# Kernel tuning notes

Hardware: AMD Instinct MI355X
Metric: run time of the kernel (lower is better)

The kernel has to match this reference:

```python
import jax, jax.numpy as jnp
import numpy as np

EPS = 1e-15
PROJ_EPS = 4e-3  # standard Poincare-ball projection epsilon (float32)


def _logmap0(x, c):
    sqrt_c = jnp.sqrt(c)
    norm = jnp.maximum(jnp.linalg.norm(x, axis=-1, keepdims=True), EPS)
    arg = jnp.clip(sqrt_c * norm, -1.0 + EPS, 1.0 - EPS)
    return x / (sqrt_c * norm) * jnp.arctanh(arg)


def _expmap0(u, c):
    sqrt_c = jnp.sqrt(c)
    norm = jnp.maximum(jnp.linalg.norm(u, axis=-1, keepdims=True), EPS)
    return jnp.tanh(sqrt_c * norm) * u / (sqrt_c * norm)


def _proj(x, c):
    maxnorm = (1.0 - PROJ_EPS) / jnp.sqrt(c)
    norm = jnp.maximum(jnp.linalg.norm(x, axis=-1, keepdims=True), EPS)
    return jnp.where(norm > maxnorm, x * (maxnorm / norm), x)


def setup_inputs() -> dict:
    key = jax.random.key(0)
    k1, k2, k3, k4 = jax.random.split(key, 4)
    N, E, F = 50000, 800000, 96
    # points strictly inside the Poincare ball
    x = 0.01 * jax.random.normal(k1, (N, F), dtype=jnp.float32)
    edge_index = jax.random.randint(k2, (2, E), 0, N, dtype=jnp.int64)
    W_up = jax.random.normal(k3, (F, F), dtype=jnp.float32) * (1.0 / np.sqrt(F))
    W_lw = jax.random.normal(k4, (1, 2 * F), dtype=jnp.float32) * (1.0 / np.sqrt(2 * F))
    return {"x": x, "edge_index": edge_index, "W_up": W_up, "W_lw": W_lw}


def reference(x, edge_index, W_up, W_lw):
    c = 1.0
    N = x.shape[0]
    row, col = edge_index[0], edge_index[1]  # source j -> target i

    x_tan = _logmap0(x, c)

    # NodeInformationScore: out = (I - D^{-1/2} A D^{-1/2}) x_tan
    ew = jnp.ones(row.shape[0], dtype=x.dtype)
    deg = jax.ops.segment_sum(ew, row, num_segments=N)
    dinv = jnp.where(deg > 0, deg, 1.0) ** -0.5
    dinv = jnp.where(deg > 0, dinv, 0.0)
    norm_e = -dinv[row] * ew * dinv[col]  # edge coefficients; self-loop coeff = 1
    info = jax.ops.segment_sum(norm_e[:, None] * x_tan[row], col, num_segments=N) + x_tan
    score = jnp.sum(jnp.abs(info), axis=1)  # [N]

    updated = jax.nn.leaky_relu(x_tan @ W_up.T, 0.01)  # [N, F]
    sum_neigh = jax.ops.segment_sum(updated[row], col, num_segments=N)

    sel = (score > 1.0).astype(x.dtype)[:, None]  # hot_prob / SEL_v
    sum_sel = jax.ops.segment_sum((sel * updated)[row], col, num_segments=N)

    w_sel = jax.nn.sigmoid(jnp.concatenate([sum_sel, sum_neigh], axis=-1) @ W_lw.T)  # [N,1]
    A_x = jax.nn.relu(jax.ops.segment_sum((w_sel * sel * updated)[row], col, num_segments=N))

    out = updated + A_x
    return _proj(_expmap0(out, c), c)
```

## Files before the change

### kernel.cpp

```cpp
#include <hip/hip_runtime.h>
#include <math.h>

#define FDIM 96
#define CAP 64
#define CAPB 5120
#define EB 8192
#define BLCAP 2048
#define T2MAX 768

typedef float f4 __attribute__((ext_vector_type(4)));
typedef unsigned u32x3 __attribute__((ext_vector_type(3)));

static __device__ __forceinline__ float wave_sum(float v) {
    for (int off = 32; off; off >>= 1) v += __shfl_xor(v, off, 64);
    return v;
}
static __device__ __forceinline__ float half_sum(float v) {
    for (int off = 16; off; off >>= 1) v += __shfl_xor(v, off, 64);
    return v;
}
static __device__ __forceinline__ float grp_sum(float v) {
    v += __shfl_xor(v, 1, 64);
    v += __shfl_xor(v, 2, 64);
    v += __shfl_xor(v, 4, 64);
    return v;
}
static __device__ __forceinline__ float bf_lo(unsigned u) { return __uint_as_float(u << 16); }
static __device__ __forceinline__ float bf_hi(unsigned u) { return __uint_as_float(u & 0xffff0000u); }
static __device__ __forceinline__ unsigned bf_rne(float f) {
    unsigned x = __float_as_uint(f);
    return (x + 0x7fffu + ((x >> 16) & 1u)) >> 16;
}
static __device__ __forceinline__ unsigned f_to_f8(float f) {
    union { _Float16 h; unsigned short u; } c;
    c.h = (_Float16)f;
    unsigned b = (unsigned)c.u + 0x80u;
    return (b >> 8) & 0xffu;
}
static __device__ __forceinline__ float f8h(unsigned hb) {
    union { unsigned short u; _Float16 h; } c;
    c.u = (unsigned short)hb;
    return (float)c.h;
}
static __device__ __forceinline__ float dot4(f4 a) {
    return a.x * a.x + a.y * a.y + a.z * a.z + a.w * a.w;
}

__global__ __launch_bounds__(512) void k_bucket_gemm(
    const int* __restrict__ row, const int* __restrict__ col,
    const float* __restrict__ x, const float* __restrict__ W,
    unsigned* __restrict__ stageC, unsigned char* __restrict__ stageR,
    int* __restrict__ fillC, int* __restrict__ fillR,
    unsigned char* __restrict__ xfb8, unsigned* __restrict__ upb,
    int n, int E, int Gbkt, int t2)
{
    __shared__ __align__(16) char shmem[FDIM * 100 * 4 + 64 * FDIM * 2];
    int t = threadIdx.x;

    if ((int)blockIdx.x < Gbkt) {
        unsigned* stC = (unsigned*)shmem;
        unsigned char* stR = (unsigned char*)(shmem + EB * 4);
        int* histC = (int*)(shmem + EB * 5);
        int* histR = histC + 256;
        int* baseC = histR + 256;
        int* baseR = baseC + 256;
        int* gbC   = baseR + 256;
        int* gbR   = gbC + 256;
        if (t < 256) { histC[t] = 0; histR[t] = 0; }
        __syncthreads();
        int e0 = (int)blockIdx.x * EB;
        unsigned pk[16];
#pragma unroll
        for (int u = 0; u < 16; ++u) {
            int e = e0 + t + u * 512;
            if (e < E) {
                unsigned c = (unsigned)col[e], r = (unsigned)row[e];
                pk[u] = (c << 16) | r;
                atomicAdd(&histC[c >> 8], 1);
                atomicAdd(&histR[r >> 8], 1);
            } else pk[u] = 0xffffffffu;
        }
        __syncthreads();
        if (t < 256) { baseC[t] = histC[t]; baseR[t] = histR[t]; }
        __syncthreads();
        for (int ofs = 1; ofs < 256; ofs <<= 1) {
            int vc = 0, vr = 0;
            if (t < 256 && t >= ofs) { vc = baseC[t - ofs]; vr = baseR[t - ofs]; }
            __syncthreads();
            if (t < 256 && t >= ofs) { baseC[t] += vc; baseR[t] += vr; }
            __syncthreads();
        }
        if (t < 256) {
            baseC[t] -= histC[t];  baseR[t] -= histR[t];
            gbC[t] = histC[t] ? atomicAdd(&fillC[t], histC[t]) : 0;
            gbR[t] = histR[t] ? atomicAdd(&fillR[t], histR[t]) : 0;
        }
        __syncthreads();
#pragma unroll
        for (int u = 0; u < 16; ++u) {
            if (pk[u] != 0xffffffffu) {
                int bc = pk[u] >> 24;
                int br = (pk[u] >> 8) & 0xff;
                int p  = atomicAdd(&baseC[bc], 1);
                stC[p] = pk[u];
                int p2 = atomicAdd(&baseR[br], 1);
                stR[p2] = (unsigned char)(pk[u] & 0xffu);
            }
        }
        __syncthreads();
        int wv = t >> 6, ln = t & 63;
        for (int b = wv; b < 256; b += 8) {
            int lenC = histC[b];
            if (lenC) {
                int s0 = baseC[b] - lenC;
                int room = CAPB - gbC[b]; if (room < 0) room = 0;
                int lim = lenC < room ? lenC : room;
                unsigned* g = stageC + (size_t)b * CAPB + gbC[b];
                for (int k = ln; k < lim; k += 64) g[k] = stC[s0 + k];
            }
            int lenR = histR[b];
            if (lenR) {
                int s1 = baseR[b] - lenR;
                int room = CAPB - gbR[b]; if (room < 0) room = 0;
                int lim = lenR < room ? lenR : room;
                unsigned char* g = stageR + (size_t)b * CAPB + gbR[b];
                for (int k = ln; k < lim; k += 64) g[k] = stR[s1 + k];
            }
        }
        return;
    }

    float* Wsf = (float*)shmem;
    unsigned short* xsb = (unsigned short*)(shmem + FDIM * 100 * 4);
    unsigned* xsb32 = (unsigned*)xsb;
    for (int idx = t; idx < FDIM * FDIM; idx += 512)
        Wsf[(idx / FDIM) * 100 + (idx % FDIM)] = W[idx];
    __syncthreads();
    int tiles = (n + 63) / 64;
    int r0 = t >> 5, c = t & 31;
    for (int tile = (int)blockIdx.x - Gbkt; tile < tiles; tile += t2) {
        int row0 = tile * 64;
#pragma unroll
        for (int rr = 0; rr < 4; ++rr) {
            int lr = r0 + rr * 16;
            int gr = row0 + lr;
            float v0 = 0.f, v1 = 0.f, v2 = 0.f;
            if (gr < n) {
                const float* xr = x + (size_t)gr * FDIM;
                v0 = xr[c]; v1 = xr[c + 32]; v2 = xr[c + 64];
            }
            float ss = half_sum(v0 * v0 + v1 * v1 + v2 * v2);
            float norm = fmaxf(sqrtf(ss), 1e-15f);
            float s = atanhf(fminf(norm, 1.0f)) / norm;
            xsb[lr * FDIM + c]      = (unsigned short)bf_rne(v0 * s);
            xsb[lr * FDIM + c + 32] = (unsigned short)bf_rne(v1 * s);
            xsb[lr * FDIM + c + 64] = (unsigned short)bf_rne(v2 * s);
        }
        __syncthreads();
        for (int idx = t; idx < 64 * 24; idx += 512) {
            int r2 = idx / 24, wq = idx % 24, g = row0 + r2;
            if (g < n) {
                unsigned p0 = xsb32[r2 * 48 + wq * 2];
                unsigned p1 = xsb32[r2 * 48 + wq * 2 + 1];
                unsigned o = f_to_f8(bf_lo(p0)) | (f_to_f8(bf_hi(p0)) << 8)
                           | (f_to_f8(bf_lo(p1)) << 16) | (f_to_f8(bf_hi(p1)) << 24);
                ((unsigned*)xfb8)[(size_t)g * 24 + wq] = o;
            }
        }
        float acc[4][3];
#pragma unroll
        for (int rr = 0; rr < 4; ++rr) { acc[rr][0] = 0.f; acc[rr][1] = 0.f; acc[rr][2] = 0.f; }
#pragma unroll 6
        for (int q = 0; q < 24; ++q) {
            f4 w0 = *(const f4*)&Wsf[c * 100 + q * 4];
            f4 w1 = *(const f4*)&Wsf[(c + 32) * 100 + q * 4];
            f4 w2 = *(const f4*)&Wsf[(c + 64) * 100 + q * 4];
#pragma unroll
            for (int rr = 0; rr < 4; ++rr) {
                uint2 xv = *(const uint2*)&xsb32[(r0 + rr * 16) * 48 + q * 2];
                float x0 = bf_lo(xv.x), x1 = bf_hi(xv.x);
                float x2 = bf_lo(xv.y), x3 = bf_hi(xv.y);
                acc[rr][0] = fmaf(x0, w0.x, fmaf(x1, w0.y, fmaf(x2, w0.z, fmaf(x3, w0.w, acc[rr][0]))));
                acc[rr][1] = fmaf(x0, w1.x, fmaf(x1, w1.y, fmaf(x2, w1.z, fmaf(x3, w1.w, acc[rr][1]))));
                acc[rr][2] = fmaf(x0, w2.x, fmaf(x1, w2.y, fmaf(x2, w2.z, fmaf(x3, w2.w, acc[rr][2]))));
            }
        }
        __syncthreads();
#pragma unroll
        for (int rr = 0; rr < 4; ++rr) {
            int lr = r0 + rr * 16;
            float a0 = acc[rr][0], a1 = acc[rr][1], a2 = acc[rr][2];
            a0 = a0 > 0.f ? a0 : 0.01f * a0;
            a1 = a1 > 0.f ? a1 : 0.01f * a1;
            a2 = a2 > 0.f ? a2 : 0.01f * a2;
            xsb[lr * FDIM + c]      = (unsigned short)bf_rne(a0);
            xsb[lr * FDIM + c + 32] = (unsigned short)bf_rne(a1);
            xsb[lr * FDIM + c + 64] = (unsigned short)bf_rne(a2);
        }
        __syncthreads();
        for (int idx = t; idx < 64 * 48; idx += 512) {
            int r2 = idx / 48, cc = idx % 48, g = row0 + r2;
            if (g < n) upb[(size_t)g * 48 + cc] = xsb32[r2 * 48 + cc];
        }
        __syncthreads();
    }
}

__global__ __launch_bounds__(512) void k_csr_deg(
    const unsigned* __restrict__ stageC, const unsigned char* __restrict__ stageR,
    const int* __restrict__ fillC, const int* __restrict__ fillR,
    float* __restrict__ dinv, int* __restrict__ cnt, unsigned short* __restrict__ srcp,
    int n, int nbuck)
{
    __shared__ __align__(16) char shmem[1024 + 256 * CAP * 2];
    int t = threadIdx.x;
    int bid = (int)blockIdx.x;

    if (bid < nbuck) {
        int* hist = (int*)shmem;
        unsigned short* comp = (unsigned short*)(shmem + 1024);
        if (t < 256) hist[t] = 0;
        __syncthreads();
        int nb = fillC[bid]; if (nb > CAPB) nb = CAPB;
        const unsigned* sc = stageC + (size_t)bid * CAPB;
        for (int k = t; k < nb; k += 512) {
            unsigned pk = sc[k];
            int cl = (pk >> 16) & 255;
            int slot = atomicAdd(&hist[cl], 1);
            if (slot < CAP) comp[cl * CAP + slot] = (unsigned short)(pk & 0xffffu);
        }
        __syncthreads();
        int node0 = bid << 8;
        if (t < 256 && node0 + t < n) cnt[node0 + t] = hist[t];
        int nnode = n - node0; if (nnode > 256) nnode = 256;
        if (nnode > 0) {
            int lim32 = nnode * (CAP / 2);
            unsigned* dst = (unsigned*)(srcp + (size_t)node0 * CAP);
            const unsigned* src = (const unsigned*)comp;
            for (int k = t; k < lim32; k += 512) dst[k] = src[k];
        }
        return;
    }
    int b = bid - nbuck;
    int* hist = (int*)shmem;
    if (t < 256) hist[t] = 0;
    __syncthreads();
    int nb = fillR[b]; if (nb > CAPB) nb = CAPB;
    const unsigned char* sr = stageR + (size_t)b * CAPB;
    for (int k = t; k < nb; k += 512) atomicAdd(&hist[sr[k]], 1);
    __syncthreads();
    int node0 = b << 8;
    if (t < 256 && node0 + t < n) {
        int d = hist[t];
        dinv[node0 + t] = d > 0 ? (float)(1.0 / sqrt((double)d)) : 0.f;
    }
}

#define DEC4(w, cf, A, B, C, D)                              \
    A = fmaf(cf, f8h(((w) & 0xffu) << 8), A);                \
    B = fmaf(cf, f8h((w) & 0xff00u), B);                     \
    C = fmaf(cf, f8h(((w) >> 8) & 0xff00u), C);              \
    D = fmaf(cf, f8h(((w) >> 16) & 0xff00u), D);

__global__ __launch_bounds__(256) void k_pass1(
    const float* __restrict__ x, const unsigned char* __restrict__ xfb8,
    const unsigned short* __restrict__ srcp, const int* __restrict__ cnt,
    const float* __restrict__ dinv, float* __restrict__ sel,
    int* __restrict__ blist, int* __restrict__ nbl, int n)
{
    int t = threadIdx.x;
    int lane = t & 63;
    int gid = lane >> 3, gl = lane & 7;
    int grp = lane & 56;
    int node = (int)blockIdx.x * 32 + (t >> 6) * 8 + gid;
    int nd = node < n ? node : 0;
    int m = cnt[nd];
    if (m > CAP) m = CAP;
    if (node >= n) m = 0;
    float di = dinv[nd];
    int jreg[8]; float cfreg[8];
#pragma unroll
    for (int s = 0; s < 8; ++s) {
        int k = s * 8 + gl;
        int j = (k < m) ? (int)srcp[(size_t)nd * CAP + k] : 0;
        jreg[s] = j;
        cfreg[s] = (k < m) ? -di * dinv[j] : 0.f;
    }
    const f4* xr = (const f4*)(x + (size_t)nd * FDIM + gl * 12);
    f4 o0 = xr[0], o1 = xr[1], o2 = xr[2];
    float ns = grp_sum(dot4(o0) + dot4(o1) + dot4(o2));
    float no = fmaxf(sqrtf(ns), 1e-15f);
    float so = atanhf(fminf(no, 1.0f)) / no;
    float a0 = o0.x*so, a1 = o0.y*so, a2 = o0.z*so, a3 = o0.w*so;
    float a4 = o1.x*so, a5 = o1.y*so, a6 = o1.z*so, a7 = o1.w*so;
    float a8 = o2.x*so, a9 = o2.y*so, a10 = o2.z*so, a11 = o2.w*so;

#pragma unroll
    for (int s = 0; s < 8; ++s) {
        if (s * 8 >= m) break;
        int jv = jreg[s]; float cfv = cfreg[s];
        u32x3 w[8]; float cf[8];
#pragma unroll
        for (int u = 0; u < 8; ++u) {
            int j = __shfl(jv, grp + u, 64);
            cf[u] = __shfl(cfv, grp + u, 64);
            w[u] = *(const u32x3*)(xfb8 + (size_t)j * 96 + gl * 12);
        }
#pragma unroll
        for (int u = 0; u < 8; ++u) {
            DEC4(w[u].x, cf[u], a0, a1, a2, a3)
            DEC4(w[u].y, cf[u], a4, a5, a6, a7)
            DEC4(w[u].z, cf[u], a8, a9, a10, a11)
        }
    }
    float sc = ((fabsf(a0) + fabsf(a1)) + (fabsf(a2) + fabsf(a3)))
             + ((fabsf(a4) + fabsf(a5)) + (fabsf(a6) + fabsf(a7)))
             + ((fabsf(a8) + fabsf(a9)) + (fabsf(a10) + fabsf(a11)));
    sc = grp_sum(sc);
    if (node < n && gl == 0) {
        sel[node] = (sc > 1.0f) ? 1.f : 0.f;
        if (sc > 0.97f && sc < 1.03f) {
            int p = atomicAdd(nbl, 1);
            if (p < BLCAP) blist[p] = node;
        }
    }
}

__global__ __launch_bounds__(256) void k_fix(
    const float* __restrict__ x, const unsigned short* __restrict__ srcp,
    const int* __restrict__ cnt, const float* __restrict__ dinv,
    const int* __restrict__ blist, const int* __restrict__ nbl,
    float* __restrict__ sel, int n)
{
    int nb = *nbl; if (nb > BLCAP) nb = BLCAP;
    int lane = threadIdx.x & 63;
    int w = ((int)blockIdx.x * 256 + (int)threadIdx.x) >> 6;
    int nw = (int)gridDim.x * 4;
    for (int idx = w; idx < nb; idx += nw) {
        int wid = blist[idx];
        float di = dinv[wid];
        int m = cnt[wid]; if (m > CAP) m = CAP;
        int jl = 0; float dvl = 0.f;
        if (lane < m) { jl = srcp[(size_t)wid * CAP + lane]; dvl = dinv[jl]; }
        float2 xo = (lane < 48) ? ((const float2*)(x + (size_t)wid * FDIM))[lane]
                                : make_float2(0.f, 0.f);
        float sso = wave_sum(xo.x * xo.x + xo.y * xo.y);
        float no = fmaxf(sqrtf(sso), 1e-15f);
        float so = atanhf(fminf(no, 1.0f)) / no;
        float fx = xo.x * so, fy = xo.y * so;
        for (int k = 0; k < m; ++k) {
            int jj = __shfl(jl, k, 64);
            float cf = -di * __shfl(dvl, k, 64);
            float2 v = (lane < 48) ? ((const float2*)(x + (size_t)jj * FDIM))[lane]
                                   : make_float2(0.f, 0.f);
            float ssj = wave_sum(v.x * v.x + v.y * v.y);
            float nj = fmaxf(sqrtf(ssj), 1e-15f);
            float sj = atanhf(fminf(nj, 1.0f)) / nj;
            fx = fmaf(cf * sj, v.x, fx);
            fy = fmaf(cf * sj, v.y, fy);
        }
        float sc = wave_sum(fabsf(fx) + fabsf(fy));
        if (lane == 0) sel[wid] = (sc > 1.0f) ? 1.f : 0.f;
    }
}

__global__ __launch_bounds__(256) void k_pass2(
    const unsigned* __restrict__ upb, const unsigned short* __restrict__ srcp,
    const int* __restrict__ cnt, const float* __restrict__ sel,
    const float* __restrict__ Wlw, float* __restrict__ wp, int n)
{
    int wid = (blockIdx.x * blockDim.x + threadIdx.x) >> 6;
    int lane = threadIdx.x & 63;
    if (wid >= n) return;
    if (sel[wid] == 0.f) { if (lane == 0) wp[wid] = 0.f; return; }
    int m = cnt[wid]; if (m > CAP) m = CAP;
    int jl = 0; float sl = 0.f;
    if (lane < m) { jl = srcp[(size_t)wid * CAP + lane]; sl = sel[jl]; }
    float snx = 0.f, sny = 0.f, ssx = 0.f, ssy = 0.f;
    for (int k = 0; k < m; ++k) {
        int j = __shfl(jl, k, 64);
        float sj = __shfl(sl, k, 64);
        if (lane < 48) {
            unsigned q = upb[(size_t)j * 48 + lane];
            float vx = bf_lo(q), vy = bf_hi(q);
            snx += vx; sny += vy;
            ssx = fmaf(sj, vx, ssx); ssy = fmaf(sj, vy, ssy);
        }
    }
    float tv = 0.f;
    if (lane < 48) {
        const float2* Wl = (const float2*)Wlw;
        float2 wsv = Wl[lane];
        float2 wnv = Wl[48 + lane];
        tv = ssx * wsv.x + ssy * wsv.y + snx * wnv.x + sny * wnv.y;
    }
    tv = wave_sum(tv);
    if (lane == 0) wp[wid] = 1.f / (1.f + expf(-tv));
}

__global__ __launch_bounds__(256) void k_pass3(
    const unsigned* __restrict__ upb,
    const unsigned short* __restrict__ srcp, const int* __restrict__ cnt,
    const float* __restrict__ wp, float* __restrict__ out, int n)
{
    int t = threadIdx.x;
    int lane = t & 63;
    int gid = lane >> 3, gl = lane & 7;
    int grp = lane & 56;
    int node = (int)blockIdx.x * 32 + (t >> 6) * 8 + gid;
    int nd = node < n ? node : 0;
    int m = cnt[nd]; if (m > CAP) m = CAP;
    if (node >= n) m = 0;
    float pl[8]; int jl[8];
#pragma unroll
    for (int s = 0; s < 8; ++s) {
        int k = s * 8 + gl;
        int j = (k < m) ? (int)srcp[(size_t)nd * CAP + k] : 0;
        jl[s] = j;
        pl[s] = (k < m) ? wp[j] : 0.f;
    }
    float any = 0.f;
#pragma unroll
    for (int s = 0; s < 8; ++s) any += pl[s];
    any = grp_sum(any);
    float b0=0.f,b1=0.f,b2=0.f,b3=0.f,b4=0.f,b5=0.f,b6=0.f,b7=0.f,b8=0.f,b9=0.f,b10=0.f,b11=0.f;
    if (any > 0.f) {
#pragma unroll
        for (int s = 0; s < 8; ++s) {
            if (s * 8 >= m) break;
            float pv = pl[s]; int jv = jl[s];
            for (int u = 0; u < 8; ++u) {
                float p = __shfl(pv, grp + u, 64);
                if (p != 0.f) {
                    int j = __shfl(jv, grp + u, 64);
                    const uint2* uj = (const uint2*)(upb + (size_t)j * 48 + gl * 6);
                    uint2 q0 = uj[0], q1 = uj[1], q2 = uj[2];
                    b0 = fmaf(p, bf_lo(q0.x), b0); b1 = fmaf(p, bf_hi(q0.x), b1);
                    b2 = fmaf(p, bf_lo(q0.y), b2); b3 = fmaf(p, bf_hi(q0.y), b3);
                    b4 = fmaf(p, bf_lo(q1.x), b4); b5 = fmaf(p, bf_hi(q1.x), b5);
                    b6 = fmaf(p, bf_lo(q1.y), b6); b7 = fmaf(p, bf_hi(q1.y), b7);
                    b8 = fmaf(p, bf_lo(q2.x), b8); b9 = fmaf(p, bf_hi(q2.x), b9);
                    b10 = fmaf(p, bf_lo(q2.y), b10); b11 = fmaf(p, bf_hi(q2.y), b11);
                }
            }
        }
    }
    b0 = fmaxf(b0, 0.f); b1 = fmaxf(b1, 0.f); b2 = fmaxf(b2, 0.f); b3 = fmaxf(b3, 0.f);
    b4 = fmaxf(b4, 0.f); b5 = fmaxf(b5, 0.f); b6 = fmaxf(b6, 0.f); b7 = fmaxf(b7, 0.f);
    b8 = fmaxf(b8, 0.f); b9 = fmaxf(b9, 0.f); b10 = fmaxf(b10, 0.f); b11 = fmaxf(b11, 0.f);
    const uint2* uo = (const uint2*)(upb + (size_t)nd * 48 + gl * 6);
    uint2 q0 = uo[0], q1 = uo[1], q2 = uo[2];
    float o0 = bf_lo(q0.x)+b0, o1 = bf_hi(q0.x)+b1, o2 = bf_lo(q0.y)+b2, o3 = bf_hi(q0.y)+b3;
    float o4 = bf_lo(q1.x)+b4, o5 = bf_hi(q1.x)+b5, o6 = bf_lo(q1.y)+b6, o7 = bf_hi(q1.y)+b7;
    float o8 = bf_lo(q2.x)+b8, o9 = bf_hi(q2.x)+b9, o10 = bf_lo(q2.y)+b10, o11 = bf_hi(q2.y)+b11;
    float ss = grp_sum(((o0*o0+o1*o1)+(o2*o2+o3*o3))+((o4*o4+o5*o5)+(o6*o6+o7*o7))
                      +((o8*o8+o9*o9)+(o10*o10+o11*o11)));
    float norm = fmaxf(sqrtf(ss), 1e-15f);
    float th = tanhf(norm);
    float s = th / norm;
    const float maxn = 1.0f - 4e-3f;
    if (th > maxn) s = maxn / norm;
    if (node < n) {
        f4* o = (f4*)(out + (size_t)node * FDIM + gl * 12);
        f4 w0, w1, w2;
        w0.x = s*o0; w0.y = s*o1; w0.z = s*o2; w0.w = s*o3;
        w1.x = s*o4; w1.y = s*o5; w1.z = s*o6; w1.w = s*o7;
        w2.x = s*o8; w2.y = s*o9; w2.z = s*o10; w2.w = s*o11;
        o[0] = w0; o[1] = w1; o[2] = w2;
    }
}

extern "C" void kernel_launch(void* const* d_in, const int* in_sizes, int n_in,
                              void* d_out, int out_size, void* d_ws, size_t ws_size,
                              hipStream_t stream) {
    const float* x   = (const float*)d_in[0];
    const int*  eidx = (const int*)d_in[1];
    const float* Wup = (const float*)d_in[2];
    const float* Wlw = (const float*)d_in[3];
    float* out = (float*)d_out;

    int N = in_sizes[0] / FDIM;
    int E = in_sizes[1] / 2;
    const int* row = eidx;
    const int* col = eidx + E;
    int nbuck = (N + 255) >> 8;

    char* ws = (char*)d_ws;
    size_t off = 0;
    auto alloc = [&](size_t bytes) {
        void* p = ws + off;
        off += (bytes + 255) & ~(size_t)255;
        return p;
    };
    unsigned char*  xfb8   = (unsigned char*)alloc((size_t)N * 96);
    unsigned*       upb    = (unsigned*)alloc((size_t)N * 48 * 4);
    unsigned*       stageC = (unsigned*)alloc((size_t)nbuck * CAPB * 4);
    unsigned char*  stageR = (unsigned char*)alloc((size_t)nbuck * CAPB);
    int*            fillC  = (int*)alloc((size_t)nbuck * 4);
    int*            fillR  = (int*)alloc((size_t)nbuck * 4);
    float*          dinv   = (float*)alloc((size_t)N * 4);
    int*            cnt    = (int*)alloc((size_t)N * 4);
    float*          sel    = (float*)alloc((size_t)N * 4);
    float*          wp     = (float*)alloc((size_t)N * 4);
    int*            blist  = (int*)alloc((size_t)BLCAP * 4);
    int*            nbl    = (int*)alloc(256);
    unsigned short* srcp   = (unsigned short*)alloc((size_t)N * CAP * 2);

    hipMemsetAsync(fillC, 0, (size_t)nbuck * 4, stream);
    hipMemsetAsync(fillR, 0, (size_t)nbuck * 4, stream);
    hipMemsetAsync(nbl, 0, 4, stream);

    int Gbkt  = (E + EB - 1) / EB;
    int tiles = (N + 63) / 64;
    int t2 = tiles < T2MAX ? tiles : T2MAX;
    dim3 blkF(512);
    dim3 blk(256);
    dim3 gridN4((N + 3) / 4);

    k_bucket_gemm<<<dim3(Gbkt + t2), blkF, 0, stream>>>(
        row, col, x, Wup, stageC, stageR, fillC, fillR, xfb8, upb, N, E, Gbkt, t2);
    k_csr_deg<<<dim3(2 * nbuck), blkF, 0, stream>>>(
        stageC, stageR, fillC, fillR, dinv, cnt, srcp, N, nbuck);
    k_pass1<<<dim3((N + 31) / 32), blk, 0, stream>>>(
        x, xfb8, srcp, cnt, dinv, sel, blist, nbl, N);
    k_fix<<<dim3(256), blk, 0, stream>>>(x, srcp, cnt, dinv, blist, nbl, sel, N);
    k_pass2<<<gridN4, blk, 0, stream>>>(upb, srcp, cnt, sel, Wlw, wp, N);
    k_pass3<<<dim3((N + 31) / 32), blk, 0, stream>>>(upb, srcp, cnt, wp, out, N);
}
```

Measured before the change: 140.2 us.

## Use bf16 MFMA for node-update GEMM and merge workspace memsets

Replaces the scalar FMA 64x96x96 GEMM tile in the fused bucket/GEMM kernel with 16x16x32 bf16 MFMA instructions, storing W as bf16 in shared memory with a padded 104-element stride. It also shrinks shared memory to the size the bucketing path needs, which may raise occupancy. The two fill-counter memsets are merged into one, and the nbl reset moves into the CSR kernel, cutting host-side launches. W is now rounded to bf16, which slightly lowers GEMM precision.

Result: faster. 120.7 us (-13.9%).

```diff
diff --git a/kernel.cpp b/kernel.cpp
--- a/kernel.cpp
+++ b/kernel.cpp
@@ -7,9 +7,13 @@
 #define EB 8192
 #define BLCAP 2048
 #define T2MAX 768
+#define XS 104
+#define XS32 52
 
 typedef float f4 __attribute__((ext_vector_type(4)));
 typedef unsigned u32x3 __attribute__((ext_vector_type(3)));
+typedef short bf16x8 __attribute__((ext_vector_type(8)));
+typedef float f32x4 __attribute__((ext_vector_type(4)));
 
 static __device__ __forceinline__ float wave_sum(float v) {
     for (int off = 32; off; off >>= 1) v += __shfl_xor(v, off, 64);
@@ -54,7 +58,7 @@
     unsigned char* __restrict__ xfb8, unsigned* __restrict__ upb,
     int n, int E, int Gbkt, int t2)
 {
-    __shared__ __align__(16) char shmem[FDIM * 100 * 4 + 64 * FDIM * 2];
+    __shared__ __align__(16) char shmem[EB * 5 + 6 * 1024];
     int t = threadIdx.x;
 
     if ((int)blockIdx.x < Gbkt) {
@@ -130,14 +134,17 @@
         return;
     }
 
-    float* Wsf = (float*)shmem;
-    unsigned short* xsb = (unsigned short*)(shmem + FDIM * 100 * 4);
+    unsigned short* Wsb = (unsigned short*)shmem;
+    unsigned short* xsb = (unsigned short*)(shmem + 96 * XS * 2);
     unsigned* xsb32 = (unsigned*)xsb;
     for (int idx = t; idx < FDIM * FDIM; idx += 512)
-        Wsf[(idx / FDIM) * 100 + (idx % FDIM)] = W[idx];
+        Wsb[(idx / FDIM) * XS + (idx % FDIM)] = (unsigned short)bf_rne(W[idx]);
     __syncthreads();
     int tiles = (n + 63) / 64;
     int r0 = t >> 5, c = t & 31;
+    int wv = t >> 6;
+    int l = t & 63;
+    int lr16 = l & 15, lk = l >> 4;
     for (int tile = (int)blockIdx.x - Gbkt; tile < tiles; tile += t2) {
         int row0 = tile * 64;
 #pragma unroll
@@ -152,55 +159,55 @@
             float ss = half_sum(v0 * v0 + v1 * v1 + v2 * v2);
             float norm = fmaxf(sqrtf(ss), 1e-15f);
             float s = atanhf(fminf(norm, 1.0f)) / norm;
-            xsb[lr * FDIM + c]      = (unsigned short)bf_rne(v0 * s);
-            xsb[lr * FDIM + c + 32] = (unsigned short)bf_rne(v1 * s);
-            xsb[lr * FDIM + c + 64] = (unsigned short)bf_rne(v2 * s);
+            xsb[lr * XS + c]      = (unsigned short)bf_rne(v0 * s);
+            xsb[lr * XS + c + 32] = (unsigned short)bf_rne(v1 * s);
+            xsb[lr * XS + c + 64] = (unsigned short)bf_rne(v2 * s);
         }
         __syncthreads();
         for (int idx = t; idx < 64 * 24; idx += 512) {
             int r2 = idx / 24, wq = idx % 24, g = row0 + r2;
             if (g < n) {
-                unsigned p0 = xsb32[r2 * 48 + wq * 2];
-                unsigned p1 = xsb32[r2 * 48 + wq * 2 + 1];
+                unsigned p0 = xsb32[r2 * XS32 + wq * 2];
+                unsigned p1 = xsb32[r2 * XS32 + wq * 2 + 1];
                 unsigned o = f_to_f8(bf_lo(p0)) | (f_to_f8(bf_hi(p0)) << 8)
                            | (f_to_f8(bf_lo(p1)) << 16) | (f_to_f8(bf_hi(p1)) << 24);
                 ((unsigned*)xfb8)[(size_t)g * 24 + wq] = o;
             }
         }
-        float acc[4][3];
-#pragma unroll
-        for (int rr = 0; rr < 4; ++rr) { acc[rr][0] = 0.f; acc[rr][1] = 0.f; acc[rr][2] = 0.f; }
-#pragma unroll 6
-        for (int q = 0; q < 24; ++q) {
-            f4 w0 = *(const f4*)&Wsf[c * 100 + q * 4];
-            f4 w1 = *(const f4*)&Wsf[(c + 32) * 100 + q * 4];
-            f4 w2 = *(const f4*)&Wsf[(c + 64) * 100 + q * 4];
-#pragma unroll
-            for (int rr = 0; rr < 4; ++rr) {
-                uint2 xv = *(const uint2*)&xsb32[(r0 + rr * 16) * 48 + q * 2];
-                float x0 = bf_lo(xv.x), x1 = bf_hi(xv.x);
-                float x2 = bf_lo(xv.y), x3 = bf_hi(xv.y);
-                acc[rr][0] = fmaf(x0, w0.x, fmaf(x1, w0.y, fmaf(x2, w0.z, fmaf(x3, w0.w, acc[rr][0]))));
-                acc[rr][1] = fmaf(x0, w1.x, fmaf(x1, w1.y, fmaf(x2, w1.z, fmaf(x3, w1.w, acc[rr][1]))));
-                acc[rr][2] = fmaf(x0, w2.x, fmaf(x1, w2.y, fmaf(x2, w2.z, fmaf(x3, w2.w, acc[rr][2]))));
-            }
-        }
-        __syncthreads();
-#pragma unroll
-        for (int rr = 0; rr < 4; ++rr) {
-            int lr = r0 + rr * 16;
-            float a0 = acc[rr][0], a1 = acc[rr][1], a2 = acc[rr][2];
-            a0 = a0 > 0.f ? a0 : 0.01f * a0;
-            a1 = a1 > 0.f ? a1 : 0.01f * a1;
-            a2 = a2 > 0.f ? a2 : 0.01f * a2;
-            xsb[lr * FDIM + c]      = (unsigned short)bf_rne(a0);
-            xsb[lr * FDIM + c + 32] = (unsigned short)bf_rne(a1);
-            xsb[lr * FDIM + c + 64] = (unsigned short)bf_rne(a2);
+        f32x4 acc0 = {0.f, 0.f, 0.f, 0.f}, acc1 = acc0, acc2 = acc0;
+#pragma unroll
+        for (int ks = 0; ks < 3; ++ks) {
+            int koff = ks * 32 + lk * 8;
+            {   int tid = wv;          int mi = tid & 3, ni = tid >> 2;
+                bf16x8 a = *(const bf16x8*)&xsb[(mi * 16 + lr16) * XS + koff];
+                bf16x8 b = *(const bf16x8*)&Wsb[(ni * 16 + lr16) * XS + koff];
+                acc0 = __builtin_amdgcn_mfma_f32_16x16x32_bf16(a, b, acc0, 0, 0, 0); }
+            {   int tid = wv + 8;      int mi = tid & 3, ni = tid >> 2;
+                bf16x8 a = *(const bf16x8*)&xsb[(mi * 16 + lr16) * XS + koff];
+                bf16x8 b = *(const bf16x8*)&Wsb[(ni * 16 + lr16) * XS + koff];
+                acc1 = __builtin_amdgcn_mfma_f32_16x16x32_bf16(a, b, acc1, 0, 0, 0); }
+            {   int tid = wv + 16;     int mi = tid & 3, ni = tid >> 2;
+                bf16x8 a = *(const bf16x8*)&xsb[(mi * 16 + lr16) * XS + koff];
+                bf16x8 b = *(const bf16x8*)&Wsb[(ni * 16 + lr16) * XS + koff];
+                acc2 = __builtin_amdgcn_mfma_f32_16x16x32_bf16(a, b, acc2, 0, 0, 0); }
+        }
+        __syncthreads();
+#pragma unroll
+        for (int tt = 0; tt < 3; ++tt) {
+            f32x4 av = tt == 0 ? acc0 : (tt == 1 ? acc1 : acc2);
+            int tid = wv + 8 * tt;
+            int mi = tid & 3, ni = tid >> 2;
+#pragma unroll
+            for (int r = 0; r < 4; ++r) {
+                float v = av[r];
+                v = v > 0.f ? v : 0.01f * v;
+                xsb[(mi * 16 + lk * 4 + r) * XS + ni * 16 + lr16] = (unsigned short)bf_rne(v);
+            }
         }
         __syncthreads();
         for (int idx = t; idx < 64 * 48; idx += 512) {
             int r2 = idx / 48, cc = idx % 48, g = row0 + r2;
-            if (g < n) upb[(size_t)g * 48 + cc] = xsb32[r2 * 48 + cc];
+            if (g < n) upb[(size_t)g * 48 + cc] = xsb32[r2 * XS32 + cc];
         }
         __syncthreads();
     }
@@ -210,11 +217,12 @@
     const unsigned* __restrict__ stageC, const unsigned char* __restrict__ stageR,
     const int* __restrict__ fillC, const int* __restrict__ fillR,
     float* __restrict__ dinv, int* __restrict__ cnt, unsigned short* __restrict__ srcp,
-    int n, int nbuck)
+    int* __restrict__ nbl, int n, int nbuck)
 {
     __shared__ __align__(16) char shmem[1024 + 256 * CAP * 2];
     int t = threadIdx.x;
     int bid = (int)blockIdx.x;
+    if (bid == 0 && t == 0) *nbl = 0;
 
     if (bid < nbuck) {
         int* hist = (int*)shmem;
@@ -496,8 +504,9 @@
     unsigned*       upb    = (unsigned*)alloc((size_t)N * 48 * 4);
     unsigned*       stageC = (unsigned*)alloc((size_t)nbuck * CAPB * 4);
     unsigned char*  stageR = (unsigned char*)alloc((size_t)nbuck * CAPB);
-    int*            fillC  = (int*)alloc((size_t)nbuck * 4);
-    int*            fillR  = (int*)alloc((size_t)nbuck * 4);
+    int*            fill2  = (int*)alloc((size_t)2 * nbuck * 4);
+    int*            fillC  = fill2;
+    int*            fillR  = fill2 + nbuck;
     float*          dinv   = (float*)alloc((size_t)N * 4);
     int*            cnt    = (int*)alloc((size_t)N * 4);
     float*          sel    = (float*)alloc((size_t)N * 4);
@@ -506,9 +515,7 @@
     int*            nbl    = (int*)alloc(256);
     unsigned short* srcp   = (unsigned short*)alloc((size_t)N * CAP * 2);
 
-    hipMemsetAsync(fillC, 0, (size_t)nbuck * 4, stream);
-    hipMemsetAsync(fillR, 0, (size_t)nbuck * 4, stream);
-    hipMemsetAsync(nbl, 0, 4, stream);
+    hipMemsetAsync(fill2, 0, (size_t)2 * nbuck * 4, stream);
 
     int Gbkt  = (E + EB - 1) / EB;
     int tiles = (N + 63) / 64;
@@ -520,7 +527,7 @@
     k_bucket_gemm<<<dim3(Gbkt + t2), blkF, 0, stream>>>(
         row, col, x, Wup, stageC, stageR, fillC, fillR, xfb8, upb, N, E, Gbkt, t2);
     k_csr_deg<<<dim3(2 * nbuck), blkF, 0, stream>>>(
-        stageC, stageR, fillC, fillR, dinv, cnt, srcp, N, nbuck);
+        stageC, stageR, fillC, fillR, dinv, cnt, srcp, nbl, N, nbuck);
     k_pass1<<<dim3((N + 31) / 32), blk, 0, stream>>>(
         x, xfb8, srcp, cnt, dinv, sel, blist, nbl, N);
     k_fix<<<dim3(256), blk, 0, stream>>>(x, srcp, cnt, dinv, blist, nbl, sel, N);
```
